# Performance work log

Hardware: AMD Instinct MI355X
Metric: run time of the kernel (lower is better)

The kernel has to match this reference:

```python
import jax, jax.numpy as jnp
import numpy as np

BATCH, GROUPS, ARITY, OUT_DIM = 1024, 512, 4, 64


def _high_order_act(X, params):
    # X: [B, G, K]; params: [G, 2**K, D]
    A_ind = jnp.argsort(X, axis=2)                                   # [B,G,K] int
    A_sort = jnp.take_along_axis(X, A_ind, axis=2)                   # sorted values
    # barycentric-style coefficients: smallest value, then successive gaps
    coef = jnp.concatenate(
        [A_sort[:, :, :1], A_sort[:, :, 1:] - A_sort[:, :, :-1]], axis=2
    )                                                                 # [B,G,K]
    # reversed cumulative sum of 2**A_ind -> vertex index into 2**K table
    pow2 = jnp.left_shift(jnp.int32(1), A_ind.astype(jnp.int32))      # [B,G,K]
    idx = jnp.flip(jnp.cumsum(jnp.flip(pow2, axis=2), axis=2), axis=2)  # [B,G,K]
    G = params.shape[0]
    g_idx = jnp.arange(G)[None, :, None]                              # [1,G,1]
    pg = params[g_idx, idx]                                           # [B,G,K,D] gather
    return jnp.einsum('bgk,bgkd->bgd', coef, pg)                      # [B,G,D]


def setup_inputs() -> dict:
    key = jax.random.key(0)
    k1, k2 = jax.random.split(key)
    X = jax.random.normal(k1, (BATCH, GROUPS, ARITY), dtype=jnp.float32)
    params = jax.random.normal(k2, (GROUPS, 2 ** ARITY, OUT_DIM), dtype=jnp.float32)
    return {"X": X, "params": params}


def reference(X, params):
    return _high_order_act(X, params)
```

## Files before the change

### kernel.cpp

```cpp
#include <hip/hip_runtime.h>

#define BATCH   1024
#define GROUPS  512
#define OUT_DIM 64

#define ROW_WORDS 68

__global__ __launch_bounds__(256) void hoact_kernel(
    const float4* __restrict__ X4,
    const float4* __restrict__ P4,
    float4*       __restrict__ O4)
{
    __shared__ float tbl[16 * ROW_WORDS];

    const int g     = blockIdx.x >> 3;
    const int chunk = blockIdx.x & 7;
    const int b0    = chunk * 128;
    const int tid   = threadIdx.x;

    {
        const float4 v = P4[g * 256 + tid];
        const int row = tid >> 4, c4 = tid & 15;
        *(float4*)&tbl[row * ROW_WORDS + c4 * 4] = v;
    }

    const int t       = tid & 7;
    const int bl_base = tid >> 3;

    float4 xv[4];
#pragma unroll
    for (int p = 0; p < 4; ++p) {
        const int b = b0 + p * 32 + bl_base;
        xv[p] = X4[b * GROUPS + g];
    }

    __syncthreads();

#pragma unroll
    for (int p = 0; p < 4; ++p) {
        const int b = b0 + p * 32 + bl_base;
        const float4 x = xv[p];

        float v0 = __uint_as_float((__float_as_uint(x.x) & ~3u) | 0u);
        float v1 = __uint_as_float((__float_as_uint(x.y) & ~3u) | 1u);
        float v2 = __uint_as_float((__float_as_uint(x.z) & ~3u) | 2u);
        float v3 = __uint_as_float((__float_as_uint(x.w) & ~3u) | 3u);

#define CSWAP(a, b_)                                 \
        {                                            \
            const float lo = fminf((a), (b_));       \
            const float hi = fmaxf((a), (b_));       \
            (a) = lo; (b_) = hi;                     \
        }
        CSWAP(v0, v1);
        CSWAP(v2, v3);
        CSWAP(v0, v2);
        CSWAP(v1, v3);
        CSWAP(v1, v2);
#undef CSWAP

        const int i1 = __float_as_uint(v1) & 3;
        const int i2 = __float_as_uint(v2) & 3;
        const int i3 = __float_as_uint(v3) & 3;

        const float c0 = v0;
        const float c1 = v1 - v0;
        const float c2 = v2 - v1;
        const float c3 = v3 - v2;

        const int e3 = 1 << i3;
        const int e2 = e3 + (1 << i2);
        const int e1 = e2 + (1 << i1);

        const float4 p0a = *(const float4*)&tbl[15 * ROW_WORDS + t * 4];
        const float4 p0b = *(const float4*)&tbl[15 * ROW_WORDS + (t + 8) * 4];
        const float4 p1a = *(const float4*)&tbl[e1 * ROW_WORDS + t * 4];
        const float4 p1b = *(const float4*)&tbl[e1 * ROW_WORDS + (t + 8) * 4];
        const float4 p2a = *(const float4*)&tbl[e2 * ROW_WORDS + t * 4];
        const float4 p2b = *(const float4*)&tbl[e2 * ROW_WORDS + (t + 8) * 4];
        const float4 p3a = *(const float4*)&tbl[e3 * ROW_WORDS + t * 4];
        const float4 p3b = *(const float4*)&tbl[e3 * ROW_WORDS + (t + 8) * 4];

        float4 oa, ob;
        oa.x = c0 * p0a.x + c1 * p1a.x + c2 * p2a.x + c3 * p3a.x;
        oa.y = c0 * p0a.y + c1 * p1a.y + c2 * p2a.y + c3 * p3a.y;
        oa.z = c0 * p0a.z + c1 * p1a.z + c2 * p2a.z + c3 * p3a.z;
        oa.w = c0 * p0a.w + c1 * p1a.w + c2 * p2a.w + c3 * p3a.w;
        ob.x = c0 * p0b.x + c1 * p1b.x + c2 * p2b.x + c3 * p3b.x;
        ob.y = c0 * p0b.y + c1 * p1b.y + c2 * p2b.y + c3 * p3b.y;
        ob.z = c0 * p0b.z + c1 * p1b.z + c2 * p2b.z + c3 * p3b.z;
        ob.w = c0 * p0b.w + c1 * p1b.w + c2 * p2b.w + c3 * p3b.w;

        const int o_idx = b * (GROUPS * 16) + g * 16 + t;
        O4[o_idx]     = oa;
        O4[o_idx + 8] = ob;
    }
}

extern "C" void kernel_launch(void* const* d_in, const int* in_sizes, int n_in,
                              void* d_out, int out_size, void* d_ws, size_t ws_size,
                              hipStream_t stream) {
    const float4* X4 = (const float4*)d_in[0];
    const float4* P4 = (const float4*)d_in[1];
    float4*       O4 = (float4*)d_out;

    const int grid = GROUPS * 8;
    hipLaunchKernelGGL(hoact_kernel, dim3(grid), dim3(256), 0, stream,
                       X4, P4, O4);
}
```

Baseline: 145.3 us.

## Tile four groups per block with contiguous 1KB output rows and prefetched X

Each block now stages the parameter tables for four consecutive groups in shared memory and covers 64 batch rows. Within a wavefront the 64 lanes write four adjacent groups times 16 float4, so each store covers one contiguous 1KB span of output instead of two split 128-byte pieces. X is software-prefetched one iteration ahead across 16 batch rows per thread. The grid halves, the shared table grows fourfold, and each thread does more serial work with fewer independent loads in flight.

After: 149.8 us. 3.1% more time.

```diff
diff --git a/kernel.cpp b/kernel.cpp
--- a/kernel.cpp
+++ b/kernel.cpp
@@ -5,46 +5,53 @@
 #define OUT_DIM 64
 
 #define ROW_WORDS 68
+#define TBL_WORDS 1092
 
 __global__ __launch_bounds__(256) void hoact_kernel(
     const float4* __restrict__ X4,
     const float4* __restrict__ P4,
     float4*       __restrict__ O4)
 {
-    __shared__ float tbl[16 * ROW_WORDS];
+    __shared__ float tbl[4 * TBL_WORDS];
 
-    const int g     = blockIdx.x >> 3;
-    const int chunk = blockIdx.x & 7;
-    const int b0    = chunk * 128;
-    const int tid   = threadIdx.x;
+    const int gq  = blockIdx.x & 127;
+    const int bc  = blockIdx.x >> 7;
+    const int g0  = gq * 4;
+    const int b0  = bc * 64;
+    const int tid = threadIdx.x;
 
-    {
-        const float4 v = P4[g * 256 + tid];
-        const int row = tid >> 4, c4 = tid & 15;
-        *(float4*)&tbl[row * ROW_WORDS + c4 * 4] = v;
+#pragma unroll
+    for (int i0 = 0; i0 < 1024; i0 += 256) {
+        const int i = i0 + tid;
+        const float4 v = P4[g0 * 256 + i];
+        const int j   = i >> 8;
+        const int rc  = i & 255;
+        const int row = rc >> 4, c4 = rc & 15;
+        *(float4*)&tbl[j * TBL_WORDS + row * ROW_WORDS + c4 * 4] = v;
     }
 
-    const int t       = tid & 7;
-    const int bl_base = tid >> 3;
-
-    float4 xv[4];
-#pragma unroll
-    for (int p = 0; p < 4; ++p) {
-        const int b = b0 + p * 32 + bl_base;
-        xv[p] = X4[b * GROUPS + g];
-    }
+    const int lane  = tid & 63;
+    const int wv    = tid >> 6;
+    const int j     = lane >> 4;
+    const int t     = lane & 15;
+    const int g     = g0 + j;
+    const int tbase = j * TBL_WORDS;
+    const int bb    = b0 + wv * 16;
 
     __syncthreads();
 
+    float4 xv = X4[bb * GROUPS + g];
+
 #pragma unroll
-    for (int p = 0; p < 4; ++p) {
-        const int b = b0 + p * 32 + bl_base;
-        const float4 x = xv[p];
+    for (int it = 0; it < 16; ++it) {
+        const int b = bb + it;
+        float4 xn;
+        if (it < 15) xn = X4[(b + 1) * GROUPS + g];
 
-        float v0 = __uint_as_float((__float_as_uint(x.x) & ~3u) | 0u);
-        float v1 = __uint_as_float((__float_as_uint(x.y) & ~3u) | 1u);
-        float v2 = __uint_as_float((__float_as_uint(x.z) & ~3u) | 2u);
-        float v3 = __uint_as_float((__float_as_uint(x.w) & ~3u) | 3u);
+        float v0 = __uint_as_float((__float_as_uint(xv.x) & ~3u) | 0u);
+        float v1 = __uint_as_float((__float_as_uint(xv.y) & ~3u) | 1u);
+        float v2 = __uint_as_float((__float_as_uint(xv.z) & ~3u) | 2u);
+        float v3 = __uint_as_float((__float_as_uint(xv.w) & ~3u) | 3u);
 
 #define CSWAP(a, b_)                                 \
         {                                            \
@@ -72,28 +79,20 @@
         const int e2 = e3 + (1 << i2);
         const int e1 = e2 + (1 << i1);
 
-        const float4 p0a = *(const float4*)&tbl[15 * ROW_WORDS + t * 4];
-        const float4 p0b = *(const float4*)&tbl[15 * ROW_WORDS + (t + 8) * 4];
-        const float4 p1a = *(const float4*)&tbl[e1 * ROW_WORDS + t * 4];
-        const float4 p1b = *(const float4*)&tbl[e1 * ROW_WORDS + (t + 8) * 4];
-        const float4 p2a = *(const float4*)&tbl[e2 * ROW_WORDS + t * 4];
-        const float4 p2b = *(const float4*)&tbl[e2 * ROW_WORDS + (t + 8) * 4];
-        const float4 p3a = *(const float4*)&tbl[e3 * ROW_WORDS + t * 4];
-        const float4 p3b = *(const float4*)&tbl[e3 * ROW_WORDS + (t + 8) * 4];
+        const float4 p0 = *(const float4*)&tbl[tbase + 15 * ROW_WORDS + t * 4];
+        const float4 p1 = *(const float4*)&tbl[tbase + e1 * ROW_WORDS + t * 4];
+        const float4 p2 = *(const float4*)&tbl[tbase + e2 * ROW_WORDS + t * 4];
+        const float4 p3 = *(const float4*)&tbl[tbase + e3 * ROW_WORDS + t * 4];
 
-        float4 oa, ob;
-        oa.x = c0 * p0a.x + c1 * p1a.x + c2 * p2a.x + c3 * p3a.x;
-        oa.y = c0 * p0a.y + c1 * p1a.y + c2 * p2a.y + c3 * p3a.y;
-        oa.z = c0 * p0a.z + c1 * p1a.z + c2 * p2a.z + c3 * p3a.z;
-        oa.w = c0 * p0a.w + c1 * p1a.w + c2 * p2a.w + c3 * p3a.w;
-        ob.x = c0 * p0b.x + c1 * p1b.x + c2 * p2b.x + c3 * p3b.x;
-        ob.y = c0 * p0b.y + c1 * p1b.y + c2 * p2b.y + c3 * p3b.y;
-        ob.z = c0 * p0b.z + c1 * p1b.z + c2 * p2b.z + c3 * p3b.z;
-        ob.w = c0 * p0b.w + c1 * p1b.w + c2 * p2b.w + c3 * p3b.w;
+        float4 o;
+        o.x = c0 * p0.x + c1 * p1.x + c2 * p2.x + c3 * p3.x;
+        o.y = c0 * p0.y + c1 * p1.y + c2 * p2.y + c3 * p3.y;
+        o.z = c0 * p0.z + c1 * p1.z + c2 * p2.z + c3 * p3.z;
+        o.w = c0 * p0.w + c1 * p1.w + c2 * p2.w + c3 * p3.w;
 
-        const int o_idx = b * (GROUPS * 16) + g * 16 + t;
-        O4[o_idx]     = oa;
-        O4[o_idx + 8] = ob;
+        O4[b * (GROUPS * 16) + g * 16 + t] = o;
+
+        xv = xn;
     }
 }
 
@@ -104,7 +103,7 @@
     const float4* P4 = (const float4*)d_in[1];
     float4*       O4 = (float4*)d_out;
 
-    const int grid = GROUPS * 8;
+    const int grid = 128 * 16;
     hipLaunchKernelGGL(hoact_kernel, dim3(grid), dim3(256), 0, stream,
                        X4, P4, O4);
 }
```
